# Optimization experiments

Measured on AMD Instinct MI355X. Metric: run time of the kernel, lower is better.

## Reference

```python
import jax, jax.numpy as jnp
import numpy as np

DIMS = 1024
HEADS = 16
HEAD_DIM = DIMS // HEADS


def setup_inputs() -> dict:
    key = jax.random.key(0)
    k_x, k_q, k_k, k_v = jax.random.split(key, 4)
    scale = 1.0 / np.sqrt(DIMS)
    return {
        "input_seq_embs": jax.random.normal(k_x, (4, 4096, DIMS), dtype=jnp.float32),
        # torch nn.Linear weights have shape (out_features, in_features)
        "W_Q": jax.random.normal(k_q, (DIMS, DIMS), dtype=jnp.float32) * scale,
        "W_K": jax.random.normal(k_k, (DIMS, DIMS), dtype=jnp.float32) * scale,
        "W_V": jax.random.normal(k_v, (DIMS, DIMS), dtype=jnp.float32) * scale,
    }


def reference(input_seq_embs, W_Q, W_K, W_V):
    B, L, d = input_seq_embs.shape
    H, hd = HEADS, HEAD_DIM
    # torch Linear: y = x @ W.T
    Q = (input_seq_embs @ W_Q.T).reshape(B, L, H, hd)
    K = (input_seq_embs @ W_K.T).reshape(B, L, H, hd)
    V = (input_seq_embs @ W_V.T).reshape(B, L, H, hd)
    # NOTE: original code does NOT move heads to dim 1, so matmuls act on
    # the trailing (H, hd) axes per token.
    # softmax(K^T) over heads axis: (B, L, hd, H)
    sK = jax.nn.softmax(jnp.swapaxes(K, -1, -2), axis=-1)
    # tran_V: (B, L, hd, hd)
    tran_V = jnp.einsum("bldh,blhe->blde", sK, V)
    # softmax(Q) over head_dim axis, then (B, L, H, hd)
    out = jnp.einsum("blhd,blde->blhe", jax.nn.softmax(Q, axis=-1), tran_V)
    return out.reshape(B, L, d)
```

## Files before the change

kernel.cpp:

```cpp
#include <hip/hip_runtime.h>
#include <stdint.h>
#include <stddef.h>

#define TOKENS 16384
#define CHUNK  8192
#define DMODEL 1024

typedef short   short8 __attribute__((ext_vector_type(8)));
typedef _Float16 half8 __attribute__((ext_vector_type(8)));
typedef float   f32x4  __attribute__((ext_vector_type(4)));
typedef unsigned short ushort_t;
typedef unsigned short us4 __attribute__((ext_vector_type(4)));

__device__ inline ushort_t f2h(float f) {
  union { _Float16 h; ushort_t u; } x; x.h = (_Float16)f; return x.u;
}
__device__ inline float h2f(ushort_t u) {
  union { _Float16 h; ushort_t u; } x; x.u = u; return (float)x.h;
}

template <typename V>
__device__ auto mfma16h_(V a, V b, f32x4 c, int)
    -> decltype(__builtin_amdgcn_mfma_f32_16x16x32_f16(a, b, c, 0, 0, 0)) {
  return __builtin_amdgcn_mfma_f32_16x16x32_f16(a, b, c, 0, 0, 0);
}
template <typename V>
__device__ f32x4 mfma16h_(V a, V b, f32x4 c, long) {
  return __builtin_amdgcn_mfma_f32_16x16x32_f16(
      __builtin_bit_cast(half8, a), __builtin_bit_cast(half8, b), c, 0, 0, 0);
}
__device__ inline f32x4 MFMA16H(short8 a, short8 b, f32x4 c) {
  return mfma16h_(a, b, c, 0);
}

__device__ inline void gload_lds16(const void* g, void* l) {
  __builtin_amdgcn_global_load_lds(
      (const __attribute__((address_space(1))) unsigned int*)g,
      (__attribute__((address_space(3))) unsigned int*)l, 16, 0, 0);
}

__device__ inline void wave_lds_fence() {
  asm volatile("s_waitcnt lgkmcnt(0)" ::: "memory");
  __builtin_amdgcn_sched_barrier(0);
}

__global__ __launch_bounds__(256) void conv_w(
    const float* __restrict__ Wq, const float* __restrict__ Wk,
    const float* __restrict__ Wv, ushort_t* __restrict__ Wh, int n4)
{
  int i = blockIdx.x * 256 + threadIdx.x;
  if (i >= n4) return;
  const float* src = (blockIdx.y == 0) ? Wq : ((blockIdx.y == 1) ? Wk : Wv);
  f32x4 x = ((const f32x4*)src)[i];
  us4 h;
  #pragma unroll
  for (int j = 0; j < 4; ++j) h[j] = f2h(x[j]);
  ((us4*)(Wh + (size_t)blockIdx.y * DMODEL * DMODEL))[i] = h;
}

__global__ __launch_bounds__(256) void conv_x(
    const float* __restrict__ src, ushort_t* __restrict__ dst, int n4)
{
  int i = blockIdx.x * 256 + threadIdx.x;
  if (i >= n4) return;
  f32x4 x = ((const f32x4*)src)[i];
  us4 h;
  #pragma unroll
  for (int j = 0; j < 4; ++j) h[j] = f2h(x[j]);
  ((us4*)dst)[i] = h;
}

__global__ __launch_bounds__(512, 2) void gemm_h(
    const ushort_t* __restrict__ Xh, const ushort_t* __restrict__ Wh,
    ushort_t* __restrict__ Y, int tokens)
{
  __shared__ ushort_t As[2][256 * 64];
  __shared__ ushort_t Bs[2][256 * 64];

  const int tid  = threadIdx.x;
  const int lane = tid & 63;
  const int wid  = tid >> 6;
  const int quad = lane >> 4;
  const int l15  = lane & 15;
  const int wm   = wid >> 2;
  const int wn   = wid & 3;

  const int m0 = blockIdx.x * 256;
  const int n0 = blockIdx.y * 256;
  const int z  = blockIdx.z;

  const ushort_t* Ag = Xh + (size_t)m0 * DMODEL;
  const ushort_t* Bg = Wh + (size_t)z * DMODEL * DMODEL + (size_t)n0 * DMODEL;
  ushort_t* Yp = Y + (size_t)z * tokens * DMODEL;

  f32x4 acc[8][4] = {};

  auto stage = [&](int t, int b) {
    const int kbase = t * 64;
    #pragma unroll
    for (int i = 0; i < 4; ++i) {
      const int c    = i * 512 + tid;
      const int row  = c >> 3;
      const int koff = (((c & 7) ^ (row & 7)) << 3);
      const size_t g = (size_t)row * DMODEL + kbase + koff;
      const int ldso = (i * 512 + wid * 64) * 16;
      gload_lds16(Ag + g, (char*)As[b] + ldso);
      gload_lds16(Bg + g, (char*)Bs[b] + ldso);
    }
  };

  stage(0, 0);
  __syncthreads();

  for (int t = 0; t < DMODEL / 64; ++t) {
    const int b = t & 1;
    if (t + 1 < DMODEL / 64) stage(t + 1, b ^ 1);

    const short8* Av = (const short8*)As[b];
    const short8* Bv = (const short8*)Bs[b];

    #pragma unroll
    for (int s = 0; s < 2; ++s) {
      short8 ah[8], bh[4];
      #pragma unroll
      for (int i = 0; i < 8; ++i) {
        const int r  = wm * 128 + i * 16 + l15;
        const int kc = s * 4 + quad;
        ah[i] = Av[r * 8 + (kc ^ (r & 7))];
      }
      #pragma unroll
      for (int j = 0; j < 4; ++j) {
        const int r  = wn * 64 + j * 16 + l15;
        const int kc = s * 4 + quad;
        bh[j] = Bv[r * 8 + (kc ^ (r & 7))];
      }
      __builtin_amdgcn_s_setprio(1);
      #pragma unroll
      for (int i = 0; i < 8; ++i) {
        #pragma unroll
        for (int j = 0; j < 4; ++j)
          acc[i][j] = MFMA16H(ah[i], bh[j], acc[i][j]);
      }
      __builtin_amdgcn_s_setprio(0);
    }
    __syncthreads();
  }

  #pragma unroll
  for (int i = 0; i < 8; ++i) {
    #pragma unroll
    for (int j = 0; j < 4; ++j) {
      #pragma unroll
      for (int r = 0; r < 4; ++r) {
        int row = m0 + wm * 128 + i * 16 + quad * 4 + r;
        int col = n0 + wn * 64 + j * 16 + l15;
        Yp[(size_t)row * DMODEL + col] = f2h(acc[i][j][r]);
      }
    }
  }
}

__global__ __launch_bounds__(256) void attn_mix(
    const ushort_t* __restrict__ QKV, float* __restrict__ Out, int tokens)
{
  __shared__ __align__(16) ushort_t V_s[4][16 * 72];
  __shared__ __align__(16) float    M_s[4][16 * 20];

  const int tid  = threadIdx.x;
  const int lane = tid & 63;
  const int wv   = tid >> 6;
  const int tok  = blockIdx.x * 4 + wv;

  const int l15  = lane & 15;
  const int quad = lane >> 4;
  const int hrow = lane >> 3;
  const int dcol = (lane & 7) * 8;

  ushort_t* Vl = V_s[wv];
  float*    Ml = M_s[wv];

  const size_t base = (size_t)tok * DMODEL;
  const size_t zstr = (size_t)tokens * DMODEL;
  const short8* Q8 = (const short8*)(QKV + base);
  const short8* K8 = (const short8*)(QKV + zstr + base);
  const short8* V8 = (const short8*)(QKV + 2 * zstr + base);

  short8 vra = V8[lane], vrb = V8[64 + lane];
  *(short8*)(Vl + hrow * 72 + dcol)       = vra;
  *(short8*)(Vl + (hrow + 8) * 72 + dcol) = vrb;

  const int fidx = l15 * 8 + quad;
  short8 qf0 = Q8[fidx], qf1 = Q8[fidx + 4];
  short8 kf0 = K8[fidx], kf1 = K8[fidx + 4];

  float eq0[8], eq1[8], ek0[8], ek1[8];
  #pragma unroll
  for (int j = 0; j < 8; ++j) {
    eq0[j] = __expf(h2f((ushort_t)qf0[j]));
    eq1[j] = __expf(h2f((ushort_t)qf1[j]));
    ek0[j] = __expf(h2f((ushort_t)kf0[j]));
    ek1[j] = __expf(h2f((ushort_t)kf1[j]));
  }

  float s0[8], s1[8];
  #pragma unroll
  for (int j = 0; j < 8; ++j) { s0[j] = ek0[j]; s1[j] = ek1[j]; }
  #pragma unroll
  for (int j = 0; j < 8; ++j) {
    s0[j] += __shfl_xor(s0[j], 1);
    s0[j] += __shfl_xor(s0[j], 2);
    s0[j] += __shfl_xor(s0[j], 4);
    s0[j] += __shfl_xor(s0[j], 8);
    s1[j] += __shfl_xor(s1[j], 1);
    s1[j] += __shfl_xor(s1[j], 2);
    s1[j] += __shfl_xor(s1[j], 4);
    s1[j] += __shfl_xor(s1[j], 8);
  }

  float sq = 0.f;
  #pragma unroll
  for (int j = 0; j < 8; ++j) sq += eq0[j] + eq1[j];
  sq += __shfl_xor(sq, 16);
  sq += __shfl_xor(sq, 32);
  const float invSq = __builtin_amdgcn_rcpf(sq);

  short8 a0v, a1v, b0v, b1v;
  #pragma unroll
  for (int j = 0; j < 8; ++j) {
    a0v[j] = (short)f2h(eq0[j] * (invSq * __builtin_amdgcn_rcpf(s0[j])));
    a1v[j] = (short)f2h(eq1[j] * (invSq * __builtin_amdgcn_rcpf(s1[j])));
    b0v[j] = (short)f2h(ek0[j]);
    b1v[j] = (short)f2h(ek1[j]);
  }

  f32x4 acc = {};
  acc = MFMA16H(a0v, b0v, acc);
  acc = MFMA16H(a1v, b1v, acc);

  #pragma unroll
  for (int r = 0; r < 4; ++r) Ml[(quad * 4 + r) * 20 + l15] = acc[r];

  wave_lds_fence();

  f32x4 m0[4], m1[4];
  #pragma unroll
  for (int j = 0; j < 4; ++j) {
    m0[j] = *(const f32x4*)(Ml + hrow * 20 + j * 4);
    m1[j] = *(const f32x4*)(Ml + (hrow + 8) * 20 + j * 4);
  }
  float o0[8] = {0.f, 0.f, 0.f, 0.f, 0.f, 0.f, 0.f, 0.f};
  float o1[8] = {0.f, 0.f, 0.f, 0.f, 0.f, 0.f, 0.f, 0.f};
  #pragma unroll
  for (int hp = 0; hp < 16; ++hp) {
    short8 vv = *(const short8*)(Vl + hp * 72 + dcol);
    const float w0 = m0[hp >> 2][hp & 3];
    const float w1 = m1[hp >> 2][hp & 3];
    #pragma unroll
    for (int j = 0; j < 8; ++j) {
      float vf = h2f((ushort_t)vv[j]);
      o0[j] += w0 * vf;
      o1[j] += w1 * vf;
    }
  }

  float* O0 = Out + base + hrow * 64 + dcol;
  float* O1 = Out + base + (hrow + 8) * 64 + dcol;
  f32x4 w;
  w[0] = o0[0]; w[1] = o0[1]; w[2] = o0[2]; w[3] = o0[3]; *(f32x4*)(O0)     = w;
  w[0] = o0[4]; w[1] = o0[5]; w[2] = o0[6]; w[3] = o0[7]; *(f32x4*)(O0 + 4) = w;
  w[0] = o1[0]; w[1] = o1[1]; w[2] = o1[2]; w[3] = o1[3]; *(f32x4*)(O1)     = w;
  w[0] = o1[4]; w[1] = o1[5]; w[2] = o1[6]; w[3] = o1[7]; *(f32x4*)(O1 + 4) = w;
}

extern "C" void kernel_launch(void* const* d_in, const int* in_sizes, int n_in,
                              void* d_out, int out_size, void* d_ws, size_t ws_size,
                              hipStream_t stream) {
  const float* X  = (const float*)d_in[0];
  const float* Wq = (const float*)d_in[1];
  const float* Wk = (const float*)d_in[2];
  const float* Wv = (const float*)d_in[3];
  float* Out = (float*)d_out;

  const size_t WSZ = (size_t)DMODEL * DMODEL;

  const size_t need1 = (3 * WSZ + (size_t)TOKENS * DMODEL * 4) * sizeof(ushort_t);
  const int    nck  = (ws_size >= need1) ? 1 : 2;
  const size_t ctok = (nck == 1) ? (size_t)TOKENS : (size_t)CHUNK;

  ushort_t* Wh = (ushort_t*)d_ws;
  ushort_t* Xh = Wh + 3 * WSZ;
  ushort_t* Yw = Xh + ctok * DMODEL;

  const int wn4 = (int)(WSZ / 4);
  dim3 gw((wn4 + 255) / 256, 3);
  conv_w<<<gw, 256, 0, stream>>>(Wq, Wk, Wv, Wh, wn4);

  const int xn4 = (int)(ctok * DMODEL / 4);
  dim3 gg((unsigned)(ctok / 256), DMODEL / 256, 3);
  for (int c = 0; c < nck; ++c) {
    conv_x<<<(xn4 + 255) / 256, 256, 0, stream>>>(X + c * ctok * DMODEL, Xh, xn4);
    gemm_h<<<gg, 512, 0, stream>>>(Xh, Wh, Yw, (int)ctok);
    attn_mix<<<(unsigned)(ctok / 4), 256, 0, stream>>>(Yw, Out + c * ctok * DMODEL, (int)ctok);
  }
}
```

Baseline: 265.5 us.

## Interleave LDS fragment reads with MFMA phases and split A/B prefetch

Restructures the projection GEMM main loop into four phases per k-tile. Each phase loads a small slice of A fragments from LDS and runs its MFMAs, while the global-to-LDS prefetch of the next A and B tiles is spread across the first two phases. It adds explicit barriers, waitcnt and sched_barrier to pin a ping-pong style schedule. The intent is better overlap of memory and matrix work with lower register pressure, at the cost of more barriers per tile.

Measured after the change: 262.9 us. Within noise of the previous version (-1.0%).

```diff
diff --git a/kernel.cpp b/kernel.cpp
--- a/kernel.cpp
+++ b/kernel.cpp
@@ -95,54 +95,80 @@
 
   f32x4 acc[8][4] = {};
 
-  auto stage = [&](int t, int b) {
+  auto stageA = [&](int t, int b) {
     const int kbase = t * 64;
     #pragma unroll
     for (int i = 0; i < 4; ++i) {
       const int c    = i * 512 + tid;
       const int row  = c >> 3;
       const int koff = (((c & 7) ^ (row & 7)) << 3);
-      const size_t g = (size_t)row * DMODEL + kbase + koff;
-      const int ldso = (i * 512 + wid * 64) * 16;
-      gload_lds16(Ag + g, (char*)As[b] + ldso);
-      gload_lds16(Bg + g, (char*)Bs[b] + ldso);
+      gload_lds16(Ag + (size_t)row * DMODEL + kbase + koff,
+                  (char*)As[b] + (i * 512 + wid * 64) * 16);
     }
   };
-
-  stage(0, 0);
+  auto stageB = [&](int t, int b) {
+    const int kbase = t * 64;
+    #pragma unroll
+    for (int i = 0; i < 4; ++i) {
+      const int c    = i * 512 + tid;
+      const int row  = c >> 3;
+      const int koff = (((c & 7) ^ (row & 7)) << 3);
+      gload_lds16(Bg + (size_t)row * DMODEL + kbase + koff,
+                  (char*)Bs[b] + (i * 512 + wid * 64) * 16);
+    }
+  };
+
+  stageA(0, 0);
+  stageB(0, 0);
+  asm volatile("s_waitcnt vmcnt(0)" ::: "memory");
   __syncthreads();
 
   for (int t = 0; t < DMODEL / 64; ++t) {
-    const int b = t & 1;
-    if (t + 1 < DMODEL / 64) stage(t + 1, b ^ 1);
-
+    const int b  = t & 1;
+    const bool pf = (t + 1 < DMODEL / 64);
     const short8* Av = (const short8*)As[b];
     const short8* Bv = (const short8*)Bs[b];
 
-    #pragma unroll
-    for (int s = 0; s < 2; ++s) {
-      short8 ah[8], bh[4];
+    short8 bh[4][2];
+    #pragma unroll
+    for (int j = 0; j < 4; ++j) {
+      const int r = wn * 64 + j * 16 + l15;
       #pragma unroll
-      for (int i = 0; i < 8; ++i) {
-        const int r  = wm * 128 + i * 16 + l15;
-        const int kc = s * 4 + quad;
-        ah[i] = Av[r * 8 + (kc ^ (r & 7))];
+      for (int s = 0; s < 2; ++s)
+        bh[j][s] = Bv[r * 8 + ((s * 4 + quad) ^ (r & 7))];
+    }
+
+    #pragma unroll
+    for (int p = 0; p < 4; ++p) {
+      short8 ah[2][2];
+      #pragma unroll
+      for (int ii = 0; ii < 2; ++ii) {
+        const int r = wm * 128 + (2 * p + ii) * 16 + l15;
+        #pragma unroll
+        for (int s = 0; s < 2; ++s)
+          ah[ii][s] = Av[r * 8 + ((s * 4 + quad) ^ (r & 7))];
       }
-      #pragma unroll
-      for (int j = 0; j < 4; ++j) {
-        const int r  = wn * 64 + j * 16 + l15;
-        const int kc = s * 4 + quad;
-        bh[j] = Bv[r * 8 + (kc ^ (r & 7))];
-      }
+      if (p == 0 && pf) stageA(t + 1, b ^ 1);
+      if (p == 1 && pf) stageB(t + 1, b ^ 1);
+
+      __builtin_amdgcn_s_barrier();
+      asm volatile("s_waitcnt lgkmcnt(0)" ::: "memory");
+      __builtin_amdgcn_sched_barrier(0);
       __builtin_amdgcn_s_setprio(1);
       #pragma unroll
-      for (int i = 0; i < 8; ++i) {
+      for (int s = 0; s < 2; ++s) {
         #pragma unroll
-        for (int j = 0; j < 4; ++j)
-          acc[i][j] = MFMA16H(ah[i], bh[j], acc[i][j]);
+        for (int ii = 0; ii < 2; ++ii) {
+          #pragma unroll
+          for (int j = 0; j < 4; ++j)
+            acc[2 * p + ii][j] = MFMA16H(ah[ii][s], bh[j][s], acc[2 * p + ii][j]);
+        }
       }
       __builtin_amdgcn_s_setprio(0);
-    }
+      __builtin_amdgcn_s_barrier();
+    }
+
+    if (pf) { asm volatile("s_waitcnt vmcnt(0)" ::: "memory"); }
     __syncthreads();
   }
 
```

## Use 4-stage K=32 LDS pipeline with explicit vmcnt waits in QKV GEMM

Applied to the files above, without the earlier changes.

The QKV projection GEMM moves from a double-buffered K=64 tile to a four-buffer K=32 ring with three tiles in flight. Hand-placed s_waitcnt vmcnt counts and one barrier per step replace the per-iteration __syncthreads. The LDS XOR swizzle is reworked for the 32-wide rows. The goal is to hide global-to-LDS load latency behind MFMA work, at the cost of more barrier steps and fragile hand-tuned wait counts.

Measured after the change: 280.8 us. +5.8%, slower.

```diff
diff --git a/kernel.cpp b/kernel.cpp
--- a/kernel.cpp
+++ b/kernel.cpp
@@ -74,8 +74,8 @@
     const ushort_t* __restrict__ Xh, const ushort_t* __restrict__ Wh,
     ushort_t* __restrict__ Y, int tokens)
 {
-  __shared__ ushort_t As[2][256 * 64];
-  __shared__ ushort_t Bs[2][256 * 64];
+  __shared__ ushort_t As[4][256 * 32];
+  __shared__ ushort_t Bs[4][256 * 32];
 
   const int tid  = threadIdx.x;
   const int lane = tid & 63;
@@ -95,13 +95,14 @@
 
   f32x4 acc[8][4] = {};
 
-  auto stage = [&](int t, int b) {
-    const int kbase = t * 64;
-    #pragma unroll
-    for (int i = 0; i < 4; ++i) {
+  auto stage = [&](int t) {
+    const int b = t & 3;
+    const int kbase = t * 32;
+    #pragma unroll
+    for (int i = 0; i < 2; ++i) {
       const int c    = i * 512 + tid;
-      const int row  = c >> 3;
-      const int koff = (((c & 7) ^ (row & 7)) << 3);
+      const int row  = c >> 2;
+      const int koff = (((c & 3) ^ ((row >> 1) & 3)) << 3);
       const size_t g = (size_t)row * DMODEL + kbase + koff;
       const int ldso = (i * 512 + wid * 64) * 16;
       gload_lds16(Ag + g, (char*)As[b] + ldso);
@@ -109,41 +110,46 @@
     }
   };
 
-  stage(0, 0);
-  __syncthreads();
-
-  for (int t = 0; t < DMODEL / 64; ++t) {
-    const int b = t & 1;
-    if (t + 1 < DMODEL / 64) stage(t + 1, b ^ 1);
-
+  stage(0);
+  stage(1);
+  stage(2);
+
+  for (int t = 0; t < DMODEL / 32; ++t) {
+    if (t < 30)       asm volatile("s_waitcnt vmcnt(8)" ::: "memory");
+    else if (t == 30) asm volatile("s_waitcnt vmcnt(4)" ::: "memory");
+    else              asm volatile("s_waitcnt vmcnt(0)" ::: "memory");
+    __builtin_amdgcn_sched_barrier(0);
+    __builtin_amdgcn_s_barrier();
+    __builtin_amdgcn_sched_barrier(0);
+
+    if (t + 3 < DMODEL / 32) stage(t + 3);
+
+    const int b = t & 3;
     const short8* Av = (const short8*)As[b];
     const short8* Bv = (const short8*)Bs[b];
 
-    #pragma unroll
-    for (int s = 0; s < 2; ++s) {
-      short8 ah[8], bh[4];
+    short8 ah[8], bh[4];
+    #pragma unroll
+    for (int f = 0; f < 8; ++f) {
+      const int r = wm * 128 + f * 16 + l15;
+      ah[f] = Av[r * 4 + (quad ^ ((r >> 1) & 3))];
+    }
+    #pragma unroll
+    for (int j = 0; j < 4; ++j) {
+      const int r = wn * 64 + j * 16 + l15;
+      bh[j] = Bv[r * 4 + (quad ^ ((r >> 1) & 3))];
+    }
+
+    asm volatile("s_waitcnt lgkmcnt(0)" ::: "memory");
+    __builtin_amdgcn_sched_barrier(0);
+    __builtin_amdgcn_s_setprio(1);
+    #pragma unroll
+    for (int f = 0; f < 8; ++f) {
       #pragma unroll
-      for (int i = 0; i < 8; ++i) {
-        const int r  = wm * 128 + i * 16 + l15;
-        const int kc = s * 4 + quad;
-        ah[i] = Av[r * 8 + (kc ^ (r & 7))];
-      }
-      #pragma unroll
-      for (int j = 0; j < 4; ++j) {
-        const int r  = wn * 64 + j * 16 + l15;
-        const int kc = s * 4 + quad;
-        bh[j] = Bv[r * 8 + (kc ^ (r & 7))];
-      }
-      __builtin_amdgcn_s_setprio(1);
-      #pragma unroll
-      for (int i = 0; i < 8; ++i) {
-        #pragma unroll
-        for (int j = 0; j < 4; ++j)
-          acc[i][j] = MFMA16H(ah[i], bh[j], acc[i][j]);
-      }
-      __builtin_amdgcn_s_setprio(0);
-    }
-    __syncthreads();
+      for (int j = 0; j < 4; ++j)
+        acc[f][j] = MFMA16H(ah[f], bh[j], acc[f][j]);
+    }
+    __builtin_amdgcn_s_setprio(0);
   }
 
   #pragma unroll
```
